# Kernel optimization log

Hardware: AMD Instinct MI355X
Metric: run time of the kernel (lower is better)

Reference implementation:

```python
import jax, jax.numpy as jnp
import numpy as np

B, T, C, H = 2, 2048, 2048, 16
DH = C // H  # 128
INNER = 4 * C  # 8192
EPS = 1e-5


def _ln(x, w, b):
    mu = jnp.mean(x, axis=-1, keepdims=True)
    var = jnp.mean((x - mu) ** 2, axis=-1, keepdims=True)
    return (x - mu) * jax.lax.rsqrt(var + EPS) * w + b


def _apply_rotary(x, cos, sin):
    # x: [B,H,T,DH]; cos/sin: [T,DH//2] broadcast over B,H
    x1 = x[..., ::2]
    x2 = x[..., 1::2]
    r = jnp.stack([x1 * cos - x2 * sin, x1 * sin + x2 * cos], axis=-1)
    return r.reshape(r.shape[:-2] + (-1,))


def setup_inputs() -> dict:
    key = jax.random.key(0)
    ks = jax.random.split(key, 8)
    std = 0.02
    x = jax.random.normal(ks[0], (B, T, C), dtype=jnp.float32)
    # RoPE tables
    inv_freq = 1.0 / (10000.0 ** (np.arange(0, DH, 2, dtype=np.float32) / DH))
    ang = np.arange(T, dtype=np.float32)[:, None] * inv_freq[None, :]  # [T, DH//2]
    cos = jnp.asarray(np.cos(ang))
    sin = jnp.asarray(np.sin(ang))
    return {
        "x": x,
        "cos": cos,
        "sin": sin,
        "ln1_w": jnp.ones((C,), jnp.float32),
        "ln1_b": jnp.zeros((C,), jnp.float32),
        "ln2_w": jnp.ones((C,), jnp.float32),
        "ln2_b": jnp.zeros((C,), jnp.float32),
        "W_qkv": jax.random.normal(ks[1], (C, 3 * C), jnp.float32) * std,
        "W_o": jax.random.normal(ks[2], (C, C), jnp.float32) * std,
        "W1": jax.random.normal(ks[3], (C, INNER), jnp.float32) * std,
        "W2": jax.random.normal(ks[4], (C, INNER), jnp.float32) * std,
        "W3": jax.random.normal(ks[5], (INNER, C), jnp.float32) * std,
    }


def reference(x, cos, sin, ln1_w, ln1_b, ln2_w, ln2_b, W_qkv, W_o, W1, W2, W3):
    # --- attention sub-block (pre-LN) ---
    a = _ln(x, ln1_w, ln1_b)
    qkv = a @ W_qkv  # [B,T,3C]
    q, k, v = jnp.split(qkv, 3, axis=-1)
    q = q.reshape(B, T, H, DH).transpose(0, 2, 1, 3)  # [B,H,T,DH]
    k = k.reshape(B, T, H, DH).transpose(0, 2, 1, 3)
    v = v.reshape(B, T, H, DH).transpose(0, 2, 1, 3)
    q = _apply_rotary(q, cos, sin)
    k = _apply_rotary(k, cos, sin)
    scores = jnp.einsum("bhtd,bhsd->bhts", q, k) / jnp.sqrt(jnp.float32(DH))
    mask = jnp.triu(jnp.full((T, T), -jnp.inf, dtype=scores.dtype), k=1)
    scores = scores + mask
    attn = jax.nn.softmax(scores, axis=-1)
    y = jnp.einsum("bhts,bhsd->bhtd", attn, v)
    y = y.transpose(0, 2, 1, 3).reshape(B, T, C) @ W_o
    x = x + y
    # --- SwiGLU MLP sub-block (pre-LN) ---
    h = _ln(x, ln2_w, ln2_b)
    m = (jax.nn.silu(h @ W1) * (h @ W2)) @ W3
    return x + m
```

## Files before the change

### kernel.cpp

```cpp
#include <hip/hip_runtime.h>
#include <hip/hip_bf16.h>
#include <cstdint>

#define DEVINL __device__ __forceinline__

using f32x4  = __attribute__((ext_vector_type(4))) float;
using short8 = __attribute__((ext_vector_type(8))) short;
using short4v = __attribute__((ext_vector_type(4))) short;

DEVINL float bf2f(__hip_bfloat16 h){ return __bfloat162float(h); }
DEVINL __hip_bfloat16 f2bf(float f){ return __float2bfloat16(f); }
DEVINL short bfbits(float f){ __hip_bfloat16 h = __float2bfloat16(f); short s; __builtin_memcpy(&s, &h, 2); return s; }
DEVINL float sb2f(short s){ uint32_t u = ((uint32_t)(uint16_t)s) << 16; float f; __builtin_memcpy(&f, &u, 4); return f; }

DEVINL void gl_lds16(const void* g, void* l){
  __builtin_amdgcn_global_load_lds((const __attribute__((address_space(1))) void*)g,
                                   (__attribute__((address_space(3))) void*)l, 16, 0, 0);
}

__global__ __launch_bounds__(256) void wtrans(const float* __restrict__ src,
                                              __hip_bfloat16* __restrict__ dst,
                                              int R, int C){
  __shared__ float tile[32][33];
  const int tr0 = blockIdx.y*32, tc0 = blockIdx.x*32;
  const int t = threadIdx.x;
  const int lr = t >> 3, lc = (t & 7) * 4;
  float4 v = *(const float4*)(src + (size_t)(tr0+lr)*C + tc0 + lc);
  tile[lr][lc] = v.x; tile[lr][lc+1] = v.y; tile[lr][lc+2] = v.z; tile[lr][lc+3] = v.w;
  __syncthreads();
  short4v o;
  o[0] = bfbits(tile[lc+0][lr]);
  o[1] = bfbits(tile[lc+1][lr]);
  o[2] = bfbits(tile[lc+2][lr]);
  o[3] = bfbits(tile[lc+3][lr]);
  *(short4v*)(dst + (size_t)(tc0+lr)*R + tr0 + lc) = o;
}

__global__ __launch_bounds__(256) void ln_k(const float* __restrict__ x,
                                            const float* __restrict__ w,
                                            const float* __restrict__ bia,
                                            __hip_bfloat16* __restrict__ out){
  const int row = blockIdx.x, t = threadIdx.x;
  const float* xr = x + (size_t)row*2048;
  float4 v0 = *(const float4*)(xr + t*4);
  float4 v1 = *(const float4*)(xr + 1024 + t*4);
  float s  = v0.x+v0.y+v0.z+v0.w + v1.x+v1.y+v1.z+v1.w;
  float ss = v0.x*v0.x+v0.y*v0.y+v0.z*v0.z+v0.w*v0.w
           + v1.x*v1.x+v1.y*v1.y+v1.z*v1.z+v1.w*v1.w;
  #pragma unroll
  for (int o=1;o<64;o<<=1){ s += __shfl_xor(s,o); ss += __shfl_xor(ss,o); }
  __shared__ float red[8];
  const int wv = t>>6, ln = t&63;
  if (ln==0){ red[wv]=s; red[4+wv]=ss; }
  __syncthreads();
  s = red[0]+red[1]+red[2]+red[3]; ss = red[4]+red[5]+red[6]+red[7];
  const float mu = s*(1.f/2048.f);
  const float inv = rsqrtf(ss*(1.f/2048.f) - mu*mu + 1e-5f);
  {
    float4 wv4 = *(const float4*)(w + t*4);
    float4 bv4 = *(const float4*)(bia + t*4);
    short4v o;
    o[0]=bfbits((v0.x-mu)*inv*wv4.x + bv4.x);
    o[1]=bfbits((v0.y-mu)*inv*wv4.y + bv4.y);
    o[2]=bfbits((v0.z-mu)*inv*wv4.z + bv4.z);
    o[3]=bfbits((v0.w-mu)*inv*wv4.w + bv4.w);
    *(short4v*)(out + (size_t)row*2048 + t*4) = o;
  }
  {
    float4 wv4 = *(const float4*)(w + 1024 + t*4);
    float4 bv4 = *(const float4*)(bia + 1024 + t*4);
    short4v o;
    o[0]=bfbits((v1.x-mu)*inv*wv4.x + bv4.x);
    o[1]=bfbits((v1.y-mu)*inv*wv4.y + bv4.y);
    o[2]=bfbits((v1.z-mu)*inv*wv4.z + bv4.z);
    o[3]=bfbits((v1.w-mu)*inv*wv4.w + bv4.w);
    *(short4v*)(out + (size_t)row*2048 + 1024 + t*4) = o;
  }
}

template<int EPI, int BM>
__global__ __launch_bounds__(512, 2) void gemm256(
    const __hip_bfloat16* __restrict__ A,
    const __hip_bfloat16* __restrict__ Bt,
    __hip_bfloat16* __restrict__ Cb,
    float* __restrict__ Cf,
    const float* __restrict__ resid,
    const __hip_bfloat16* __restrict__ emul,
    int M, int N, int K, int NTN)
{
  constexpr int MF     = BM/32;
  constexpr int NA     = BM/64;
  constexpr int ABYTES = BM*128;
  constexpr int TILEB  = ABYTES + 32768;
  constexpr int NLD    = NA + 4;
  extern __shared__ char smem[];
  const int tid = threadIdx.x, lane = tid & 63, wave = tid >> 6;
  const int l15 = lane & 15, l4 = lane >> 4;
  const int wm = wave >> 2, wn = wave & 3;

  const int nwg = gridDim.x;
  const int id  = blockIdx.x;
  const int swz = (id & 7) * (nwg >> 3) + (id >> 3);
  const int by = swz / NTN, bx = swz % NTN;
  const int row0 = by * BM, col0 = bx * 256;

  const __hip_bfloat16* gptr[NLD];
  int ldsoff[NLD];
  #pragma unroll
  for (int g = 0; g < NLD; ++g){
    const int gg = (g < NA) ? g : g - NA;
    const int r    = gg*64 + (tid >> 3);
    const int colp = (tid & 7) * 16;
    const int coll = colp ^ ((r & 7) << 4);
    if (g < NA) gptr[g] = A  + (size_t)(row0 + r)*K + (coll >> 1);
    else        gptr[g] = Bt + (size_t)(col0 + r)*K + (coll >> 1);
    ldsoff[g] = (g < NA ? 0 : ABYTES) + gg*8192 + tid*16;
  }
  auto STAGE = [&](int bufc, int ktile){
    #pragma unroll
    for (int g = 0; g < NLD; ++g)
      gl_lds16(gptr[g] + (size_t)ktile*64, smem + bufc + ldsoff[g]);
  };

  const int swzm = (l15 & 7) << 4;
  const int aRow = (wm*(BM/2) + l15) * 128;
  const int bRow = ABYTES + (wn*64 + l15) * 128;
  const int colT0 = (l4*16) ^ swzm;
  const int colT1 = (64 + l4*16) ^ swzm;

  f32x4 acc[MF][4] = {};
  const int NT = K >> 6;

  STAGE(0, 0);
  STAGE(TILEB, 1);
  __builtin_amdgcn_sched_barrier(0);
  if constexpr (BM == 256) asm volatile("s_waitcnt vmcnt(8)" ::: "memory");
  else                     asm volatile("s_waitcnt vmcnt(6)" ::: "memory");
  __builtin_amdgcn_s_barrier();
  __builtin_amdgcn_sched_barrier(0);

  for (int t = 0; t < NT; ++t){
    const int bufc = (t & 1) * TILEB;
    #pragma unroll
    for (int ks = 0; ks < 2; ++ks){
      const int ct = (ks == 0) ? colT0 : colT1;
      short8 a[MF], b[4];
      #pragma unroll
      for (int m = 0; m < MF; ++m) a[m] = *(const short8*)(smem + bufc + aRow + m*2048 + ct);
      #pragma unroll
      for (int n = 0; n < 4; ++n) b[n] = *(const short8*)(smem + bufc + bRow + n*2048 + ct);
      __builtin_amdgcn_s_setprio(1);
      #pragma unroll
      for (int m = 0; m < MF; ++m)
        #pragma unroll
        for (int n = 0; n < 4; ++n)
          acc[m][n] = __builtin_amdgcn_mfma_f32_16x16x32_bf16(a[m], b[n], acc[m][n], 0, 0, 0);
      __builtin_amdgcn_s_setprio(0);
    }
    __builtin_amdgcn_sched_barrier(0);
    __builtin_amdgcn_s_barrier();
    __builtin_amdgcn_sched_barrier(0);
    if (t + 2 < NT){
      STAGE(bufc, t + 2);
      __builtin_amdgcn_sched_barrier(0);
      if constexpr (BM == 256) asm volatile("s_waitcnt vmcnt(8)" ::: "memory");
      else                     asm volatile("s_waitcnt vmcnt(6)" ::: "memory");
    } else {
      asm volatile("s_waitcnt vmcnt(0)" ::: "memory");
    }
    __builtin_amdgcn_s_barrier();
    __builtin_amdgcn_sched_barrier(0);
  }

  #pragma unroll
  for (int m = 0; m < MF; ++m){
    const int r0 = row0 + wm*(BM/2) + m*16 + l4*4;
    #pragma unroll
    for (int n = 0; n < 4; ++n){
      const int c = col0 + wn*64 + n*16 + l15;
      #pragma unroll
      for (int j = 0; j < 4; ++j){
        const size_t idx = (size_t)(r0 + j)*N + c;
        const float v = acc[m][n][j];
        if constexpr (EPI == 1)      Cf[idx] = v + resid[idx];
        else if constexpr (EPI == 2) Cb[idx] = f2bf(v / (1.f + __expf(-v)));
        else if constexpr (EPI == 3) Cb[idx] = f2bf(v * bf2f(emul[idx]));
        else                         Cb[idx] = f2bf(v);
      }
    }
  }
}

__global__ __launch_bounds__(256) void ropepack(
    const __hip_bfloat16* __restrict__ qkv, const float* __restrict__ cosT, const float* __restrict__ sinT,
    __hip_bfloat16* __restrict__ Qo, __hip_bfloat16* __restrict__ Ko, __hip_bfloat16* __restrict__ Vo)
{
  __shared__ short vt[128][72];
  const int bh = blockIdx.y, b = bh>>4, h = bh&15;
  const int t0 = blockIdx.x*64, tid = threadIdx.x;
  const int tr = tid>>2, q4 = tid&3;
  const int tg = t0 + tr;
  const __hip_bfloat16* base = qkv + ((size_t)(b*2048 + tg))*6144 + h*128;
  const int pp0 = q4*16;
  float cs[16], sn[16];
  #pragma unroll
  for (int i=0;i<4;i++){
    float4 c4 = *(const float4*)(cosT + (size_t)tg*64 + pp0 + i*4);
    float4 s4 = *(const float4*)(sinT + (size_t)tg*64 + pp0 + i*4);
    cs[i*4+0]=c4.x; cs[i*4+1]=c4.y; cs[i*4+2]=c4.z; cs[i*4+3]=c4.w;
    sn[i*4+0]=s4.x; sn[i*4+1]=s4.y; sn[i*4+2]=s4.z; sn[i*4+3]=s4.w;
  }
  #pragma unroll
  for (int qk=0; qk<2; ++qk){
    const __hip_bfloat16* src = base + qk*2048;
    __hip_bfloat16* dst = (qk==0 ? Qo : Ko) + ((size_t)bh*2048 + tg)*128 + pp0*2;
    short8 ov[4];
    short* o = (short*)ov;
    #pragma unroll
    for (int i=0;i<4;i++){
      short8 v = *(const short8*)(src + pp0*2 + i*8);
      #pragma unroll
      for (int j=0;j<4;j++){
        float xe = sb2f(v[2*j]), xo = sb2f(v[2*j+1]);
        float c = cs[4*i+j], s = sn[4*i+j];
        o[8*i+2*j]   = bfbits(xe*c - xo*s);
        o[8*i+2*j+1] = bfbits(xe*s + xo*c);
      }
    }
    #pragma unroll
    for (int i=0;i<4;i++) *(short8*)(dst + i*8) = ov[i];
  }
  const __hip_bfloat16* vsrc = base + 4096;
  const int vc0 = q4*32;
  #pragma unroll
  for (int i=0;i<4;i++){
    short8 v = *(const short8*)(vsrc + vc0 + i*8);
    #pragma unroll
    for (int j=0;j<8;j++) vt[vc0+i*8+j][tr] = v[j];
  }
  __syncthreads();
  const int d = tid>>1, th0 = (tid&1)*32;
  __hip_bfloat16* vdst = Vo + ((size_t)bh*128 + d)*2048 + t0 + th0;
  #pragma unroll
  for (int i=0;i<4;i++)
    *(short8*)(vdst + i*8) = *(const short8*)(&vt[d][th0 + i*8]);
}

__global__ __launch_bounds__(512, 2) void attn_k(
    const __hip_bfloat16* __restrict__ Q,
    const __hip_bfloat16* __restrict__ K,
    const __hip_bfloat16* __restrict__ Vt,
    __hip_bfloat16* __restrict__ Y)
{
  extern __shared__ char lds[];
  const int bh = blockIdx.x, b = bh>>4, h = bh&15;
  const int by = blockIdx.y;
  const int qtA = 15 - 2*by, qtB = 2*by;
  const int tid = threadIdx.x, lane = tid&63, wave = tid>>6;
  const int qt = (wave < 4) ? qtA : qtB;
  const int qbase = qt*128 + (wave&3)*32;
  const int qmax = (qtA > qtB) ? qtA : qtB;
  const int nsteps = 2*qmax + 2;
  const __hip_bfloat16* Qh = Q + (size_t)bh*2048*128;
  const __hip_bfloat16* Kh = K + (size_t)bh*2048*128;
  const __hip_bfloat16* Vh = Vt + (size_t)bh*128*2048;
  char* plbase = lds + 65536 + wave*4608;
  const int l15 = lane & 15, l4 = lane >> 4;
  const int swzm = (l15 & 7) << 4;

  const int krA = tid >> 4;  const int kjA = (tid & 15) * 16;
  const size_t ksrcA = (size_t)krA*128 + ((kjA ^ ((krA & 7) << 4)) >> 1);
  const size_t ksrcB = (size_t)(krA+32)*128 + ((kjA ^ ((krA & 7) << 4)) >> 1);
  const int vrA = tid >> 3;  const int vjA = (tid & 7) * 16;
  const size_t vsrcA = (size_t)vrA*2048 + ((vjA ^ ((vrA & 7) << 4)) >> 1);
  const size_t vsrcB = (size_t)(vrA+64)*2048 + ((vjA ^ ((vrA & 7) << 4)) >> 1);
  auto STAGE = [&](int buf, int kv0){
    char* kb = lds + buf*16384;
    char* vb = lds + 32768 + buf*16384;
    gl_lds16(Kh + (size_t)kv0*128 + ksrcA, kb + tid*16);
    gl_lds16(Kh + (size_t)kv0*128 + ksrcB, kb + 8192 + tid*16);
    gl_lds16(Vh + kv0 + vsrcA, vb + tid*16);
    gl_lds16(Vh + kv0 + vsrcB, vb + 8192 + tid*16);
  };

  short8 qf[2][4];
  #pragma unroll
  for (int m=0;m<2;m++)
    #pragma unroll
    for (int kc=0;kc<4;kc++)
      qf[m][kc] = *(const short8*)(Qh + (size_t)(qbase + m*16 + l15)*128 + kc*32 + l4*8);

  short8 of;
  #pragma unroll
  for (int i=0;i<8;i++) of[i] = (l15==0) ? (short)0x3F80 : (short)0;

  f32x4 accO[2][9] = {};
  float mrow[2][4];
  #pragma unroll
  for (int m=0;m<2;m++)
    #pragma unroll
    for (int j=0;j<4;j++) mrow[m][j] = -1e30f;
  const float scale = 0.08838834764831845f;

  STAGE(0, 0);
  STAGE(1, 64);
  __builtin_amdgcn_sched_barrier(0);
  asm volatile("s_waitcnt vmcnt(4)" ::: "memory");
  __builtin_amdgcn_s_barrier();
  __builtin_amdgcn_sched_barrier(0);

  for (int s = 0; s < nsteps; ++s){
    const int kv0 = s*64;
    const char* kb = lds + (s&1)*16384;
    const char* vb = lds + 32768 + (s&1)*16384;
    if (kv0 <= qbase){
      const bool diag = (kv0 + 64 > qbase);
      const int kvrel = kv0 - qbase;
      f32x4 sc[2][4] = {};
      #pragma unroll
      for (int n=0;n<4;n++){
        short8 kf[4];
        #pragma unroll
        for (int kc=0;kc<4;kc++)
          kf[kc] = *(const short8*)(kb + (n*16 + l15)*256 + ((kc*64 + l4*16) ^ swzm));
        #pragma unroll
        for (int m=0;m<2;m++)
          #pragma unroll
          for (int kc=0;kc<4;kc++)
            sc[m][n] = __builtin_amdgcn_mfma_f32_16x16x32_bf16(qf[m][kc], kf[kc], sc[m][n], 0,0,0);
      }
      float alpha_[2][4];
      #pragma unroll
      for (int m=0;m<2;m++)
        #pragma unroll
        for (int j=0;j<4;j++){
          const int qr = 16*m + 4*l4 + j;
          float a[4];
          #pragma unroll
          for (int n=0;n<4;n++){
            a[n] = sc[m][n][j]*scale;
            if (diag && (kvrel + n*16 + l15 > qr)) a[n] = -1e30f;
          }
          float mx = fmaxf(fmaxf(a[0],a[1]), fmaxf(a[2],a[3]));
          #pragma unroll
          for (int o=1;o<16;o<<=1) mx = fmaxf(mx, __shfl_xor(mx, o));
          const float mn = fmaxf(mrow[m][j], mx);
          const float al = __expf(mrow[m][j] - mn);
          mrow[m][j] = mn;
          alpha_[m][j] = al;
          __hip_bfloat16* pr = (__hip_bfloat16*)(plbase + qr*144) + l15;
          #pragma unroll
          for (int n=0;n<4;n++) pr[n*16] = f2bf(__expf(a[n] - mn));
        }
      #pragma unroll
      for (int m=0;m<2;m++)
        #pragma unroll
        for (int db=0;db<9;db++)
          #pragma unroll
          for (int j=0;j<4;j++)
            accO[m][db][j] *= alpha_[m][j];
      asm volatile("s_waitcnt lgkmcnt(0)" ::: "memory");
      __builtin_amdgcn_sched_barrier(0);
      short8 pa[2][2];
      #pragma unroll
      for (int m=0;m<2;m++)
        #pragma unroll
        for (int ks=0;ks<2;ks++)
          pa[m][ks] = *(const short8*)(plbase + (m*16 + l15)*144 + ks*64 + l4*16);
      #pragma unroll
      for (int db=0;db<8;db++){
        #pragma unroll
        for (int ks=0;ks<2;ks++){
          short8 vf = *(const short8*)(vb + (db*16 + l15)*128 + ((ks*64 + l4*16) ^ swzm));
          #pragma unroll
          for (int m=0;m<2;m++)
            accO[m][db] = __builtin_amdgcn_mfma_f32_16x16x32_bf16(pa[m][ks], vf, accO[m][db], 0,0,0);
        }
      }
      #pragma unroll
      for (int ks=0;ks<2;ks++)
        #pragma unroll
        for (int m=0;m<2;m++)
          accO[m][8] = __builtin_amdgcn_mfma_f32_16x16x32_bf16(pa[m][ks], of, accO[m][8], 0,0,0);
    }
    __builtin_amdgcn_sched_barrier(0);
    __builtin_amdgcn_s_barrier();
    __builtin_amdgcn_sched_barrier(0);
    if (s + 2 < nsteps){
      STAGE(s&1, (s+2)*64);
      __builtin_amdgcn_sched_barrier(0);
      asm volatile("s_waitcnt vmcnt(4)" ::: "memory");
    } else {
      asm volatile("s_waitcnt vmcnt(0)" ::: "memory");
    }
    __builtin_amdgcn_s_barrier();
    __builtin_amdgcn_sched_barrier(0);
  }

  #pragma unroll
  for (int m=0;m<2;m++){
    float lr[4];
    #pragma unroll
    for (int j=0;j<4;j++) lr[j] = __shfl(accO[m][8][j], l4*16);
    #pragma unroll
    for (int db=0;db<8;db++)
      #pragma unroll
      for (int j=0;j<4;j++){
        const int tg = qbase + 16*m + 4*l4 + j;
        const int d  = 16*db + l15;
        Y[((size_t)b*2048 + tg)*2048 + h*128 + d] = f2bf(accO[m][db][j] / lr[j]);
      }
  }
}

extern "C" void kernel_launch(void* const* d_in, const int* in_sizes, int n_in,
                              void* d_out, int out_size, void* d_ws, size_t ws_size,
                              hipStream_t stream)
{
  const float* x    = (const float*)d_in[0];
  const float* cosT = (const float*)d_in[1];
  const float* sinT = (const float*)d_in[2];
  const float* ln1w = (const float*)d_in[3];
  const float* ln1b = (const float*)d_in[4];
  const float* ln2w = (const float*)d_in[5];
  const float* ln2b = (const float*)d_in[6];
  const float* Wqkv = (const float*)d_in[7];
  const float* Wo   = (const float*)d_in[8];
  const float* W1   = (const float*)d_in[9];
  const float* W2   = (const float*)d_in[10];
  const float* W3   = (const float*)d_in[11];
  float* out = (float*)d_out;

  if (ws_size < 150994944) return;
  char* ws = (char*)d_ws;
  __hip_bfloat16* WT   = (__hip_bfloat16*)(ws);
  __hip_bfloat16* abf  = (__hip_bfloat16*)(ws + 33554432);
  __hip_bfloat16* qkvb = (__hip_bfloat16*)(ws + 50331648);
  __hip_bfloat16* Yb   = (__hip_bfloat16*)(ws + 50331648);
  __hip_bfloat16* sub  = (__hip_bfloat16*)(ws + 50331648);
  __hip_bfloat16* Qb   = (__hip_bfloat16*)(ws + 100663296);
  __hip_bfloat16* Kb   = (__hip_bfloat16*)(ws + 117440512);
  __hip_bfloat16* Vtb  = (__hip_bfloat16*)(ws + 134217728);
  float*          x2   = out;

  hipFuncSetAttribute(reinterpret_cast<const void*>(&gemm256<4,256>),
                      hipFuncAttributeMaxDynamicSharedMemorySize, 131072);
  hipFuncSetAttribute(reinterpret_cast<const void*>(&gemm256<2,256>),
                      hipFuncAttributeMaxDynamicSharedMemorySize, 131072);
  hipFuncSetAttribute(reinterpret_cast<const void*>(&gemm256<3,256>),
                      hipFuncAttributeMaxDynamicSharedMemorySize, 131072);
  hipFuncSetAttribute(reinterpret_cast<const void*>(&gemm256<1,128>),
                      hipFuncAttributeMaxDynamicSharedMemorySize, 98304);
  hipFuncSetAttribute(reinterpret_cast<const void*>(&attn_k),
                      hipFuncAttributeMaxDynamicSharedMemorySize, 102400);

  ln_k<<<4096,256,0,stream>>>(x, ln1w, ln1b, abf);
  wtrans<<<dim3(192,64),256,0,stream>>>(Wqkv, WT, 2048, 6144);
  gemm256<4,256><<<384,512,131072,stream>>>(abf, WT, qkvb, nullptr, nullptr, nullptr, 4096, 6144, 2048, 24);
  ropepack<<<dim3(32,32),256,0,stream>>>(qkvb, cosT, sinT, Qb, Kb, Vtb);
  attn_k<<<dim3(32,8),512,102400,stream>>>(Qb, Kb, Vtb, Yb);
  wtrans<<<dim3(64,64),256,0,stream>>>(Wo, WT, 2048, 2048);
  gemm256<1,128><<<256,512,98304,stream>>>(Yb, WT, nullptr, x2, x, nullptr, 4096, 2048, 2048, 8);
  ln_k<<<4096,256,0,stream>>>(x2, ln2w, ln2b, abf);
  wtrans<<<dim3(256,64),256,0,stream>>>(W1, WT, 2048, 8192);
  gemm256<2,256><<<512,512,131072,stream>>>(abf, WT, sub, nullptr, nullptr, nullptr, 4096, 8192, 2048, 32);
  wtrans<<<dim3(256,64),256,0,stream>>>(W2, WT, 2048, 8192);
  gemm256<3,256><<<512,512,131072,stream>>>(abf, WT, sub, nullptr, nullptr, sub, 4096, 8192, 2048, 32);
  wtrans<<<dim3(64,256),256,0,stream>>>(W3, WT, 8192, 2048);
  gemm256<1,128><<<256,512,98304,stream>>>(sub, WT, nullptr, out, x2, nullptr, 4096, 2048, 8192, 8);
}
```

Measured before the change: 813.3 us.

## Restructure GEMM main loop into finer-grained interleaved load/MFMA phases

Replaces the GEMM's two-stage whole-tile prefetch with a schedule that splits each K-tile into two 32-wide halves and each wave's M fragments into two halves. It interleaves global-to-LDS loads for the next tile between MFMA phases, with barriers between phases, in the style of an 8-phase ping-pong schedule. The shared-memory layout is repacked so two rows share a 128-byte line with XOR swizzling. The goal is to overlap memory traffic with matrix math more evenly. In exchange it adds many more barriers per tile and shortens the prefetch distance from two tiles to one.

Result: slower. 836.7 us (+2.9%).

```diff
diff --git a/kernel.cpp b/kernel.cpp
--- a/kernel.cpp
+++ b/kernel.cpp
@@ -79,7 +79,7 @@
 }
 
 template<int EPI, int BM>
-__global__ __launch_bounds__(512, 2) void gemm256(
+__global__ __launch_bounds__(512, 2) void gemm8p(
     const __hip_bfloat16* __restrict__ A,
     const __hip_bfloat16* __restrict__ Bt,
     __hip_bfloat16* __restrict__ Cb,
@@ -88,11 +88,12 @@
     const __hip_bfloat16* __restrict__ emul,
     int M, int N, int K, int NTN)
 {
-  constexpr int MF     = BM/32;
-  constexpr int NA     = BM/64;
-  constexpr int ABYTES = BM*128;
-  constexpr int TILEB  = ABYTES + 32768;
-  constexpr int NLD    = NA + 4;
+  constexpr int MF    = BM/32;
+  constexpr int MH    = MF/2;
+  constexpr int LA    = BM/128;
+  constexpr int AH    = BM*64;
+  constexpr int BH    = 16384;
+  constexpr int TILEB = 2*AH + 2*BH;
   extern __shared__ char smem[];
   const int tid = threadIdx.x, lane = tid & 63, wave = tid >> 6;
   const int l15 = lane & 15, l4 = lane >> 4;
@@ -104,72 +105,110 @@
   const int by = swz / NTN, bx = swz % NTN;
   const int row0 = by * BM, col0 = bx * 256;
 
-  const __hip_bfloat16* gptr[NLD];
-  int ldsoff[NLD];
-  #pragma unroll
-  for (int g = 0; g < NLD; ++g){
-    const int gg = (g < NA) ? g : g - NA;
-    const int r    = gg*64 + (tid >> 3);
-    const int colp = (tid & 7) * 16;
-    const int coll = colp ^ ((r & 7) << 4);
-    if (g < NA) gptr[g] = A  + (size_t)(row0 + r)*K + (coll >> 1);
-    else        gptr[g] = Bt + (size_t)(col0 + r)*K + (coll >> 1);
-    ldsoff[g] = (g < NA ? 0 : ABYTES) + gg*8192 + tid*16;
-  }
-  auto STAGE = [&](int bufc, int ktile){
-    #pragma unroll
-    for (int g = 0; g < NLD; ++g)
-      gl_lds16(gptr[g] + (size_t)ktile*64, smem + bufc + ldsoff[g]);
+  const __hip_bfloat16* srcA[LA]; int dstA[LA];
+  #pragma unroll
+  for (int g = 0; g < LA; ++g){
+    const int c = g*512 + tid, p = c >> 3, slot = c & 7;
+    const int clog = (slot ^ (p & 7)) << 4;
+    const int r = 2*p + (clog >> 6), kb = clog & 63;
+    srcA[g] = A + (size_t)(row0 + r)*K + (kb >> 1);
+    dstA[g] = c*16;
+  }
+  const __hip_bfloat16* srcB[2]; int dstB[2];
+  #pragma unroll
+  for (int g = 0; g < 2; ++g){
+    const int c = g*512 + tid, p = c >> 3, slot = c & 7;
+    const int clog = (slot ^ (p & 7)) << 4;
+    const int r = 2*p + (clog >> 6), kb = clog & 63;
+    srcB[g] = Bt + (size_t)(col0 + r)*K + (kb >> 1);
+    dstB[g] = c*16;
+  }
+  auto STA = [&](int bufc, int kt, int ks){
+    #pragma unroll
+    for (int g = 0; g < LA; ++g)
+      gl_lds16(srcA[g] + kt*64 + ks*32, smem + bufc + ks*AH + dstA[g]);
   };
-
-  const int swzm = (l15 & 7) << 4;
-  const int aRow = (wm*(BM/2) + l15) * 128;
-  const int bRow = ABYTES + (wn*64 + l15) * 128;
-  const int colT0 = (l4*16) ^ swzm;
-  const int colT1 = (64 + l4*16) ^ swzm;
+  auto STB = [&](int bufc, int kt, int ks){
+    #pragma unroll
+    for (int g = 0; g < 2; ++g)
+      gl_lds16(srcB[g] + kt*64 + ks*32, smem + bufc + 2*AH + ks*BH + dstB[g]);
+  };
+
+  int offA[MF], offB[4];
+  #pragma unroll
+  for (int m = 0; m < MF; ++m){
+    const int r = wm*(BM/2) + m*16 + l15, p = r >> 1;
+    offA[m] = p*128 + (((((r&1)<<6) | (l4<<4))) ^ ((p & 7) << 4));
+  }
+  #pragma unroll
+  for (int n = 0; n < 4; ++n){
+    const int r = wn*64 + n*16 + l15, p = r >> 1;
+    offB[n] = p*128 + (((((r&1)<<6) | (l4<<4))) ^ ((p & 7) << 4));
+  }
 
   f32x4 acc[MF][4] = {};
   const int NT = K >> 6;
 
-  STAGE(0, 0);
-  STAGE(TILEB, 1);
+  STA(0, 0, 0); STB(0, 0, 0); STA(0, 0, 1); STB(0, 0, 1);
   __builtin_amdgcn_sched_barrier(0);
-  if constexpr (BM == 256) asm volatile("s_waitcnt vmcnt(8)" ::: "memory");
-  else                     asm volatile("s_waitcnt vmcnt(6)" ::: "memory");
+  if constexpr (LA == 2) asm volatile("s_waitcnt vmcnt(4)" ::: "memory");
+  else                   asm volatile("s_waitcnt vmcnt(3)" ::: "memory");
   __builtin_amdgcn_s_barrier();
   __builtin_amdgcn_sched_barrier(0);
 
   for (int t = 0; t < NT; ++t){
     const int bufc = (t & 1) * TILEB;
+    const int obuf = bufc ^ TILEB;
+    const bool pf = (t + 1 < NT);
+    short8 a[MH], b[4], a2[MH];
     #pragma unroll
     for (int ks = 0; ks < 2; ++ks){
-      const int ct = (ks == 0) ? colT0 : colT1;
-      short8 a[MF], b[4];
-      #pragma unroll
-      for (int m = 0; m < MF; ++m) a[m] = *(const short8*)(smem + bufc + aRow + m*2048 + ct);
-      #pragma unroll
-      for (int n = 0; n < 4; ++n) b[n] = *(const short8*)(smem + bufc + bRow + n*2048 + ct);
+      const char* ab = smem + bufc + ks*AH;
+      const char* bb = smem + bufc + 2*AH + ks*BH;
+      #pragma unroll
+      for (int i = 0; i < MH; ++i) a[i] = *(const short8*)(ab + offA[i]);
+      #pragma unroll
+      for (int n = 0; n < 4; ++n)  b[n] = *(const short8*)(bb + offB[n]);
+      if (pf) STA(obuf, t + 1, ks);
+      __builtin_amdgcn_sched_barrier(0);
+      __builtin_amdgcn_s_barrier();
+      asm volatile("s_waitcnt lgkmcnt(0)" ::: "memory");
+      __builtin_amdgcn_sched_barrier(0);
       __builtin_amdgcn_s_setprio(1);
       #pragma unroll
-      for (int m = 0; m < MF; ++m)
+      for (int m = 0; m < MH; ++m)
         #pragma unroll
         for (int n = 0; n < 4; ++n)
           acc[m][n] = __builtin_amdgcn_mfma_f32_16x16x32_bf16(a[m], b[n], acc[m][n], 0, 0, 0);
       __builtin_amdgcn_s_setprio(0);
+      __builtin_amdgcn_sched_barrier(0);
+      __builtin_amdgcn_s_barrier();
+      __builtin_amdgcn_sched_barrier(0);
+      #pragma unroll
+      for (int i = 0; i < MH; ++i) a2[i] = *(const short8*)(ab + offA[MH + i]);
+      if (pf){
+        STB(obuf, t + 1, ks);
+        __builtin_amdgcn_sched_barrier(0);
+        if constexpr (LA == 2) asm volatile("s_waitcnt vmcnt(4)" ::: "memory");
+        else                   asm volatile("s_waitcnt vmcnt(3)" ::: "memory");
+      } else {
+        asm volatile("s_waitcnt vmcnt(0)" ::: "memory");
+      }
+      __builtin_amdgcn_sched_barrier(0);
+      __builtin_amdgcn_s_barrier();
+      asm volatile("s_waitcnt lgkmcnt(0)" ::: "memory");
+      __builtin_amdgcn_sched_barrier(0);
+      __builtin_amdgcn_s_setprio(1);
+      #pragma unroll
+      for (int m = 0; m < MH; ++m)
+        #pragma unroll
+        for (int n = 0; n < 4; ++n)
+          acc[MH + m][n] = __builtin_amdgcn_mfma_f32_16x16x32_bf16(a2[m], b[n], acc[MH + m][n], 0, 0, 0);
+      __builtin_amdgcn_s_setprio(0);
+      __builtin_amdgcn_sched_barrier(0);
+      __builtin_amdgcn_s_barrier();
+      __builtin_amdgcn_sched_barrier(0);
     }
-    __builtin_amdgcn_sched_barrier(0);
-    __builtin_amdgcn_s_barrier();
-    __builtin_amdgcn_sched_barrier(0);
-    if (t + 2 < NT){
-      STAGE(bufc, t + 2);
-      __builtin_amdgcn_sched_barrier(0);
-      if constexpr (BM == 256) asm volatile("s_waitcnt vmcnt(8)" ::: "memory");
-      else                     asm volatile("s_waitcnt vmcnt(6)" ::: "memory");
-    } else {
-      asm volatile("s_waitcnt vmcnt(0)" ::: "memory");
-    }
-    __builtin_amdgcn_s_barrier();
-    __builtin_amdgcn_sched_barrier(0);
   }
 
   #pragma unroll
@@ -443,29 +482,29 @@
   __hip_bfloat16* Vtb  = (__hip_bfloat16*)(ws + 134217728);
   float*          x2   = out;
 
-  hipFuncSetAttribute(reinterpret_cast<const void*>(&gemm256<4,256>),
+  hipFuncSetAttribute(reinterpret_cast<const void*>(&gemm8p<4,256>),
                       hipFuncAttributeMaxDynamicSharedMemorySize, 131072);
-  hipFuncSetAttribute(reinterpret_cast<const void*>(&gemm256<2,256>),
+  hipFuncSetAttribute(reinterpret_cast<const void*>(&gemm8p<2,256>),
                       hipFuncAttributeMaxDynamicSharedMemorySize, 131072);
-  hipFuncSetAttribute(reinterpret_cast<const void*>(&gemm256<3,256>),
+  hipFuncSetAttribute(reinterpret_cast<const void*>(&gemm8p<3,256>),
                       hipFuncAttributeMaxDynamicSharedMemorySize, 131072);
-  hipFuncSetAttribute(reinterpret_cast<const void*>(&gemm256<1,128>),
+  hipFuncSetAttribute(reinterpret_cast<const void*>(&gemm8p<1,128>),
                       hipFuncAttributeMaxDynamicSharedMemorySize, 98304);
   hipFuncSetAttribute(reinterpret_cast<const void*>(&attn_k),
                       hipFuncAttributeMaxDynamicSharedMemorySize, 102400);
 
   ln_k<<<4096,256,0,stream>>>(x, ln1w, ln1b, abf);
   wtrans<<<dim3(192,64),256,0,stream>>>(Wqkv, WT, 2048, 6144);
-  gemm256<4,256><<<384,512,131072,stream>>>(abf, WT, qkvb, nullptr, nullptr, nullptr, 4096, 6144, 2048, 24);
+  gemm8p<4,256><<<384,512,131072,stream>>>(abf, WT, qkvb, nullptr, nullptr, nullptr, 4096, 6144, 2048, 24);
   ropepack<<<dim3(32,32),256,0,stream>>>(qkvb, cosT, sinT, Qb, Kb, Vtb);
   attn_k<<<dim3(32,8),512,102400,stream>>>(Qb, Kb, Vtb, Yb);
   wtrans<<<dim3(64,64),256,0,stream>>>(Wo, WT, 2048, 2048);
-  gemm256<1,128><<<256,512,98304,stream>>>(Yb, WT, nullptr, x2, x, nullptr, 4096, 2048, 2048, 8);
+  gemm8p<1,128><<<256,512,98304,stream>>>(Yb, WT, nullptr, x2, x, nullptr, 4096, 2048, 2048, 8);
   ln_k<<<4096,256,0,stream>>>(x2, ln2w, ln2b, abf);
   wtrans<<<dim3(256,64),256,0,stream>>>(W1, WT, 2048, 8192);
-  gemm256<2,256><<<512,512,131072,stream>>>(abf, WT, sub, nullptr, nullptr, nullptr, 4096, 8192, 2048, 32);
+  gemm8p<2,256><<<512,512,131072,stream>>>(abf, WT, sub, nullptr, nullptr, nullptr, 4096, 8192, 2048, 32);
   wtrans<<<dim3(256,64),256,0,stream>>>(W2, WT, 2048, 8192);
-  gemm256<3,256><<<512,512,131072,stream>>>(abf, WT, sub, nullptr, nullptr, sub, 4096, 8192, 2048, 32);
+  gemm8p<3,256><<<512,512,131072,stream>>>(abf, WT, sub, nullptr, nullptr, sub, 4096, 8192, 2048, 32);
   wtrans<<<dim3(64,256),256,0,stream>>>(W3, WT, 8192, 2048);
-  gemm256<1,128><<<256,512,98304,stream>>>(sub, WT, nullptr, out, x2, nullptr, 4096, 2048, 8192, 8);
-}
+  gemm8p<1,128><<<256,512,98304,stream>>>(sub, WT, nullptr, out, x2, nullptr, 4096, 2048, 8192, 8);
+}
```

## Restructure GEMM into 4-stage pipeline with 32-wide K tiles and XCD tile mapping

Applied to the files above, without the earlier changes.

The bf16 GEMM now uses 32-element K tiles held in a 4-deep LDS ring, prefetching three tiles ahead, instead of 64-element tiles double-buffered two ahead. LDS rows shrink to 64 bytes with a matching 4-way XOR swizzle, and per-fragment read offsets are precomputed. Work-group to tile mapping now gives each XCD a contiguous band of output columns, which should improve L2 reuse of the weight matrix. The aim is deeper latency hiding of global loads, at the cost of twice as many barriers per unit of K and less MFMA work between synchronisations.

Result: slower. 868.0 us (+6.7%).

```diff
diff --git a/kernel.cpp b/kernel.cpp
--- a/kernel.cpp
+++ b/kernel.cpp
@@ -79,7 +79,7 @@
 }
 
 template<int EPI, int BM>
-__global__ __launch_bounds__(512, 2) void gemm256(
+__global__ __launch_bounds__(512, 2) void gemmq(
     const __hip_bfloat16* __restrict__ A,
     const __hip_bfloat16* __restrict__ Bt,
     __hip_bfloat16* __restrict__ Cb,
@@ -88,51 +88,60 @@
     const __hip_bfloat16* __restrict__ emul,
     int M, int N, int K, int NTN)
 {
-  constexpr int MF     = BM/32;
-  constexpr int NA     = BM/64;
-  constexpr int ABYTES = BM*128;
-  constexpr int TILEB  = ABYTES + 32768;
-  constexpr int NLD    = NA + 4;
+  constexpr int MF    = BM/32;
+  constexpr int LA    = BM/128;
+  constexpr int ABY   = BM*64;
+  constexpr int TILEB = ABY + 16384;
   extern __shared__ char smem[];
   const int tid = threadIdx.x, lane = tid & 63, wave = tid >> 6;
   const int l15 = lane & 15, l4 = lane >> 4;
   const int wm = wave >> 2, wn = wave & 3;
 
-  const int nwg = gridDim.x;
   const int id  = blockIdx.x;
-  const int swz = (id & 7) * (nwg >> 3) + (id >> 3);
-  const int by = swz / NTN, bx = swz % NTN;
+  const int xcd = id & 7, jj = id >> 3, cpx = NTN >> 3;
+  const int bx = xcd*cpx + jj % cpx, by = jj / cpx;
   const int row0 = by * BM, col0 = bx * 256;
 
-  const __hip_bfloat16* gptr[NLD];
-  int ldsoff[NLD];
-  #pragma unroll
-  for (int g = 0; g < NLD; ++g){
-    const int gg = (g < NA) ? g : g - NA;
-    const int r    = gg*64 + (tid >> 3);
-    const int colp = (tid & 7) * 16;
-    const int coll = colp ^ ((r & 7) << 4);
-    if (g < NA) gptr[g] = A  + (size_t)(row0 + r)*K + (coll >> 1);
-    else        gptr[g] = Bt + (size_t)(col0 + r)*K + (coll >> 1);
-    ldsoff[g] = (g < NA ? 0 : ABYTES) + gg*8192 + tid*16;
-  }
-  auto STAGE = [&](int bufc, int ktile){
-    #pragma unroll
-    for (int g = 0; g < NLD; ++g)
-      gl_lds16(gptr[g] + (size_t)ktile*64, smem + bufc + ldsoff[g]);
+  const __hip_bfloat16* srcA[LA]; int dstA[LA];
+  #pragma unroll
+  for (int g = 0; g < LA; ++g){
+    const int c = g*512 + tid, r = c >> 2, s = c & 3;
+    const int colb = (s << 4) ^ ((r & 3) << 4);
+    srcA[g] = A + (size_t)(row0 + r)*K + (colb >> 1);
+    dstA[g] = c*16;
+  }
+  const __hip_bfloat16* srcB[2]; int dstB[2];
+  #pragma unroll
+  for (int g = 0; g < 2; ++g){
+    const int c = g*512 + tid, r = c >> 2, s = c & 3;
+    const int colb = (s << 4) ^ ((r & 3) << 4);
+    srcB[g] = Bt + (size_t)(col0 + r)*K + (colb >> 1);
+    dstB[g] = c*16;
+  }
+  auto STAGE = [&](int bi, int kt){
+    char* base = smem + bi*TILEB;
+    #pragma unroll
+    for (int g = 0; g < LA; ++g) gl_lds16(srcA[g] + kt*32, base + dstA[g]);
+    #pragma unroll
+    for (int g = 0; g < 2; ++g)  gl_lds16(srcB[g] + kt*32, base + ABY + dstB[g]);
   };
 
-  const int swzm = (l15 & 7) << 4;
-  const int aRow = (wm*(BM/2) + l15) * 128;
-  const int bRow = ABYTES + (wn*64 + l15) * 128;
-  const int colT0 = (l4*16) ^ swzm;
-  const int colT1 = (64 + l4*16) ^ swzm;
+  int offA[MF], offB[4];
+  #pragma unroll
+  for (int m = 0; m < MF; ++m){
+    const int r = wm*(BM/2) + m*16 + l15;
+    offA[m] = r*64 + ((l4*16) ^ ((r & 3) << 4));
+  }
+  #pragma unroll
+  for (int n = 0; n < 4; ++n){
+    const int r = wn*64 + n*16 + l15;
+    offB[n] = r*64 + ((l4*16) ^ ((r & 3) << 4));
+  }
 
   f32x4 acc[MF][4] = {};
-  const int NT = K >> 6;
-
-  STAGE(0, 0);
-  STAGE(TILEB, 1);
+  const int NT = K >> 5;
+
+  STAGE(0, 0); STAGE(1, 1); STAGE(2, 2);
   __builtin_amdgcn_sched_barrier(0);
   if constexpr (BM == 256) asm volatile("s_waitcnt vmcnt(8)" ::: "memory");
   else                     asm volatile("s_waitcnt vmcnt(6)" ::: "memory");
@@ -140,28 +149,24 @@
   __builtin_amdgcn_sched_barrier(0);
 
   for (int t = 0; t < NT; ++t){
-    const int bufc = (t & 1) * TILEB;
-    #pragma unroll
-    for (int ks = 0; ks < 2; ++ks){
-      const int ct = (ks == 0) ? colT0 : colT1;
-      short8 a[MF], b[4];
-      #pragma unroll
-      for (int m = 0; m < MF; ++m) a[m] = *(const short8*)(smem + bufc + aRow + m*2048 + ct);
-      #pragma unroll
-      for (int n = 0; n < 4; ++n) b[n] = *(const short8*)(smem + bufc + bRow + n*2048 + ct);
-      __builtin_amdgcn_s_setprio(1);
-      #pragma unroll
-      for (int m = 0; m < MF; ++m)
-        #pragma unroll
-        for (int n = 0; n < 4; ++n)
-          acc[m][n] = __builtin_amdgcn_mfma_f32_16x16x32_bf16(a[m], b[n], acc[m][n], 0, 0, 0);
-      __builtin_amdgcn_s_setprio(0);
-    }
+    const char* base = smem + (t & 3)*TILEB;
+    short8 a[MF], b[4];
+    #pragma unroll
+    for (int m = 0; m < MF; ++m) a[m] = *(const short8*)(base + offA[m]);
+    #pragma unroll
+    for (int n = 0; n < 4; ++n)  b[n] = *(const short8*)(base + ABY + offB[n]);
+    __builtin_amdgcn_s_setprio(1);
+    #pragma unroll
+    for (int m = 0; m < MF; ++m)
+      #pragma unroll
+      for (int n = 0; n < 4; ++n)
+        acc[m][n] = __builtin_amdgcn_mfma_f32_16x16x32_bf16(a[m], b[n], acc[m][n], 0, 0, 0);
+    __builtin_amdgcn_s_setprio(0);
     __builtin_amdgcn_sched_barrier(0);
     __builtin_amdgcn_s_barrier();
     __builtin_amdgcn_sched_barrier(0);
-    if (t + 2 < NT){
-      STAGE(bufc, t + 2);
+    if (t + 3 < NT){
+      STAGE((t + 3) & 3, t + 3);
       __builtin_amdgcn_sched_barrier(0);
       if constexpr (BM == 256) asm volatile("s_waitcnt vmcnt(8)" ::: "memory");
       else                     asm volatile("s_waitcnt vmcnt(6)" ::: "memory");
@@ -443,29 +448,29 @@
   __hip_bfloat16* Vtb  = (__hip_bfloat16*)(ws + 134217728);
   float*          x2   = out;
 
-  hipFuncSetAttribute(reinterpret_cast<const void*>(&gemm256<4,256>),
+  hipFuncSetAttribute(reinterpret_cast<const void*>(&gemmq<4,256>),
                       hipFuncAttributeMaxDynamicSharedMemorySize, 131072);
-  hipFuncSetAttribute(reinterpret_cast<const void*>(&gemm256<2,256>),
+  hipFuncSetAttribute(reinterpret_cast<const void*>(&gemmq<2,256>),
                       hipFuncAttributeMaxDynamicSharedMemorySize, 131072);
-  hipFuncSetAttribute(reinterpret_cast<const void*>(&gemm256<3,256>),
+  hipFuncSetAttribute(reinterpret_cast<const void*>(&gemmq<3,256>),
                       hipFuncAttributeMaxDynamicSharedMemorySize, 131072);
-  hipFuncSetAttribute(reinterpret_cast<const void*>(&gemm256<1,128>),
+  hipFuncSetAttribute(reinterpret_cast<const void*>(&gemmq<1,128>),
                       hipFuncAttributeMaxDynamicSharedMemorySize, 98304);
   hipFuncSetAttribute(reinterpret_cast<const void*>(&attn_k),
                       hipFuncAttributeMaxDynamicSharedMemorySize, 102400);
 
   ln_k<<<4096,256,0,stream>>>(x, ln1w, ln1b, abf);
   wtrans<<<dim3(192,64),256,0,stream>>>(Wqkv, WT, 2048, 6144);
-  gemm256<4,256><<<384,512,131072,stream>>>(abf, WT, qkvb, nullptr, nullptr, nullptr, 4096, 6144, 2048, 24);
+  gemmq<4,256><<<384,512,131072,stream>>>(abf, WT, qkvb, nullptr, nullptr, nullptr, 4096, 6144, 2048, 24);
   ropepack<<<dim3(32,32),256,0,stream>>>(qkvb, cosT, sinT, Qb, Kb, Vtb);
   attn_k<<<dim3(32,8),512,102400,stream>>>(Qb, Kb, Vtb, Yb);
   wtrans<<<dim3(64,64),256,0,stream>>>(Wo, WT, 2048, 2048);
-  gemm256<1,128><<<256,512,98304,stream>>>(Yb, WT, nullptr, x2, x, nullptr, 4096, 2048, 2048, 8);
+  gemmq<1,128><<<256,512,98304,stream>>>(Yb, WT, nullptr, x2, x, nullptr, 4096, 2048, 2048, 8);
   ln_k<<<4096,256,0,stream>>>(x2, ln2w, ln2b, abf);
   wtrans<<<dim3(256,64),256,0,stream>>>(W1, WT, 2048, 8192);
-  gemm256<2,256><<<512,512,131072,stream>>>(abf, WT, sub, nullptr, nullptr, nullptr, 4096, 8192, 2048, 32);
+  gemmq<2,256><<<512,512,131072,stream>>>(abf, WT, sub, nullptr, nullptr, nullptr, 4096, 8192, 2048, 32);
   wtrans<<<dim3(256,64),256,0,stream>>>(W2, WT, 2048, 8192);
-  gemm256<3,256><<<512,512,131072,stream>>>(abf, WT, sub, nullptr, nullptr, sub, 4096, 8192, 2048, 32);
+  gemmq<3,256><<<512,512,131072,stream>>>(abf, WT, sub, nullptr, nullptr, sub, 4096, 8192, 2048, 32);
   wtrans<<<dim3(64,256),256,0,stream>>>(W3, WT, 8192, 2048);
-  gemm256<1,128><<<256,512,98304,stream>>>(sub, WT, nullptr, out, x2, nullptr, 4096, 2048, 8192, 8);
-}
+  gemmq<1,128><<<256,512,98304,stream>>>(sub, WT, nullptr, out, x2, nullptr, 4096, 2048, 8192, 8);
+}
```
